# Performance work log

Hardware: AMD Instinct MI355X
Metric: run time of the kernel (lower is better)

The kernel has to match this reference:

```python
import jax, jax.numpy as jnp
import numpy as np


def _l2norm(x, eps=1e-6):
    return x / jnp.sqrt(jnp.sum(x * x, axis=-1, keepdims=True) + eps)


def setup_inputs() -> dict:
    key = jax.random.key(0)
    k1, k2, k3, k4 = jax.random.split(key, 4)
    b, h, L, dk, dv = 2, 8, 4096, 128, 128
    q = jax.random.normal(k1, (b, h, L, dk), jnp.float32)
    k = jax.random.normal(k2, (b, h, L, dk), jnp.float32)
    v = jax.random.normal(k3, (b, h, L, dv), jnp.float32)
    beta = jax.random.uniform(k4, (b, h, L), jnp.float32)  # sigmoid(b_proj) in module -> (0,1)
    return {"q": q, "k": k, "v": v, "beta": beta, "chunk_size": 32}


def _delta_rule_chunkwise(q, k, v, beta, chunk_size):
    b, h, L, dk = q.shape
    dv = v.shape[-1]
    c = chunk_size
    pad = (-L) % c
    if pad:
        q = jnp.pad(q, ((0, 0), (0, 0), (0, pad), (0, 0)))
        k = jnp.pad(k, ((0, 0), (0, 0), (0, pad), (0, 0)))
        v = jnp.pad(v, ((0, 0), (0, 0), (0, pad), (0, 0)))
        beta = jnp.pad(beta, ((0, 0), (0, 0), (0, pad)))
    Lp = L + pad
    n = Lp // c

    q = _l2norm(q)
    k = _l2norm(k)
    v = v * beta[..., None]
    kb = k * beta[..., None]

    # (b,h,n,c,d)
    resh = lambda t: t.reshape(b, h, n, c, t.shape[-1])
    q, k, v, kb = resh(q), resh(k), resh(v), resh(kb)

    tri = jnp.triu(jnp.ones((c, c), bool), 0)        # upper incl diag
    tri_s = jnp.triu(jnp.ones((c, c), bool), 1)      # strict upper

    # forward substitution: inv = (I + strictly-lower(k_beta k^T))^{-1}-style recurrence
    inv = -jnp.einsum('bhncd,bhned->bhnce', kb, k)
    inv = jnp.where(tri, 0.0, inv)
    for i in range(1, c):  # fixed small chunk_size loop (c=32)
        upd = jnp.einsum('bhnk,bhnkj->bhnj', inv[..., i, :], inv[..., :, :i])
        inv = inv.at[..., i, :i].add(upd)
    inv = inv + jnp.eye(c, dtype=inv.dtype)

    u = inv @ v    # (b,h,n,c,dv)
    w = inv @ kb   # (b,h,n,c,dk)

    # chunk-recurrent state scan over the n blocks
    qs = jnp.moveaxis(q, 2, 0)
    ks = jnp.moveaxis(k, 2, 0)
    us = jnp.moveaxis(u, 2, 0)
    ws = jnp.moveaxis(w, 2, 0)
    S0 = jnp.zeros((b, h, dk, dv), q.dtype)

    def step(S, blk):
        q_i, k_i, u_i, w_i = blk
        attn = jnp.einsum('bhcd,bhed->bhce', q_i, k_i)
        attn = jnp.where(tri_s, 0.0, attn)                       # causal within chunk
        u_i = u_i - jnp.einsum('bhcd,bhde->bhce', w_i, S)
        o_i = jnp.einsum('bhcd,bhde->bhce', q_i, S) + jnp.einsum('bhce,bhed->bhcd', attn, u_i)
        S = S + jnp.einsum('bhcd,bhce->bhde', k_i, u_i)
        return S, o_i

    S, out = jax.lax.scan(step, S0, (qs, ks, us, ws))
    out = jnp.moveaxis(out, 0, 2).reshape(b, h, Lp, dv)[:, :, :L]
    return out, S


def reference(q, k, v, beta, chunk_size):
    return _delta_rule_chunkwise(q, k, v, beta, int(chunk_size))
```

## Files before the change

kernel.cpp:

```cpp
#include <hip/hip_runtime.h>
#include <cstddef>

#define BH   16
#define LSEQ 4096
#define DK   128
#define DV   128
#define C    32
#define NCH  128
#define DVB  16
#define NDVB 8
#define PP   136
#define PC   40
#define PS   136
#define AP   33

#define RECSZ 22528
#define OQ    0
#define OWH   4096
#define OWL   8192
#define OKTH  12288
#define OKTL  16384
#define OATH  20480
#define OATL  21504

typedef __attribute__((ext_vector_type(4))) float f32x4;
typedef __attribute__((ext_vector_type(8))) short short8;
typedef __attribute__((ext_vector_type(4))) short s16x4;

__device__ inline unsigned split_bf16(float x) {
    unsigned u = __builtin_bit_cast(unsigned, x);
    unsigned r = u + 0x7fffu + ((u >> 16) & 1u);
    unsigned h = r >> 16;
    float hf = __builtin_bit_cast(float, r & 0xffff0000u);
    float res = x - hf;
    unsigned u2 = __builtin_bit_cast(unsigned, res);
    unsigned r2 = u2 + 0x7fffu + ((u2 >> 16) & 1u);
    return (h << 16) | (r2 >> 16);
}
__device__ inline short hi_bf16(float x) {
    unsigned u = __builtin_bit_cast(unsigned, x);
    return (short)((u + 0x7fffu + ((u >> 16) & 1u)) >> 16);
}
__device__ inline short trunc_bf16(float x) {
    return (short)(__builtin_bit_cast(unsigned, x) >> 16);
}

__device__ inline short8 fld(const short* P, int row0, int pitch, int k0, int lane) {
    return *(const short8*)(P + (row0 + (lane & 15)) * pitch + k0 + ((lane >> 4) << 3));
}
__device__ inline short8 fldz128(const short* P, int row0, int ks, int lane) {
    int row = row0 + (lane & 15);
    int c = ks * 4 + (lane >> 4);
    return *(const short8*)(P + row * 128 + ((c ^ (row & 7)) << 3));
}
__device__ inline short8 fldz32(const short* P, int row0, int lane) {
    int row = row0 + (lane & 15);
    int c = lane >> 4;
    return *(const short8*)(P + row * 32 + ((c ^ (row & 3)) << 3));
}
__device__ inline f32x4 mf(short8 a, short8 b, f32x4 c) {
    return __builtin_amdgcn_mfma_f32_16x16x32_bf16(a, b, c, 0, 0, 0);
}
__device__ inline void build_ifrags(int lane, short8& Iev, short8& Iod) {
    int n = lane & 15, q = lane >> 4;
#pragma unroll
    for (int j = 0; j < 8; ++j) {
        Iev[j] = (q * 8 + j == n)      ? (short)0x3F80 : (short)0;
        Iod[j] = (q * 8 + j == n + 16) ? (short)0x3F80 : (short)0;
    }
}
__device__ inline void store8_z128(short* Pg, int row, int col0, s16x4 v) {
    int c = col0 >> 3;
    *(s16x4*)(Pg + row * 128 + ((c ^ (row & 7)) << 3) + (col0 & 7)) = v;
}
__device__ inline void store8_z32(short* Pg, int row, int col0, s16x4 v) {
    int c = col0 >> 3;
    *(s16x4*)(Pg + row * 32 + ((c ^ (row & 3)) << 3) + (col0 & 7)) = v;
}
__device__ inline void dma1k(const short* g, short* l, int lane) {
    __builtin_amdgcn_global_load_lds(
        (const __attribute__((address_space(1))) unsigned int*)(g + lane * 8),
        (__attribute__((address_space(3))) unsigned int*)l, 16, 0, 0);
}

__global__ __launch_bounds__(256) void k_prep(const float* __restrict__ Q,
                                              const float* __restrict__ K,
                                              const float* __restrict__ V,
                                              const float* __restrict__ Beta,
                                              short* __restrict__ RECg,
                                              float* __restrict__ Uws) {
    __shared__ short knh[C * PP], knl[C * PP], vh[C * PP], vl[C * PP], qh[C * PP];
    __shared__ short knTh[DK * PC], knTl[DK * PC], vTh[DK * PC], vTl[DK * PC];
    __shared__ short Th[C * PC], Tl[C * PC];
    __shared__ float A[C * AP];
    __shared__ float sbeta[C];

    const int t = threadIdx.x, lane = t & 63, wv = t >> 6;
    const int quad = (t >> 4) & 3, l15 = t & 15;
    const int g = blockIdx.x;
    const size_t base = (size_t)g * (C * DK);
    short* rec = RECg + (size_t)g * RECSZ;
    short8 Iev, Iod;
    build_ifrags(lane, Iev, Iod);

    if (t < C) sbeta[t] = Beta[(size_t)(g >> 7) * LSEQ + (size_t)(g & 127) * C + t];

    const int sr = t >> 3, sc = (t & 7) * 16;
    f32x4 kk[4], vv[4], qq[4];
#pragma unroll
    for (int g4 = 0; g4 < 4; ++g4) {
        kk[g4] = *(const f32x4*)(K + base + 16 * t + 4 * g4);
        vv[g4] = *(const f32x4*)(V + base + 16 * t + 4 * g4);
        qq[g4] = *(const f32x4*)(Q + base + 16 * t + 4 * g4);
    }
    float ssk = 0.f, ssq = 0.f;
#pragma unroll
    for (int g4 = 0; g4 < 4; ++g4) {
#pragma unroll
        for (int e = 0; e < 4; ++e) {
            ssk += kk[g4][e] * kk[g4][e];
            ssq += qq[g4][e] * qq[g4][e];
        }
    }
    ssk += __shfl_xor(ssk, 1); ssk += __shfl_xor(ssk, 2); ssk += __shfl_xor(ssk, 4);
    ssq += __shfl_xor(ssq, 1); ssq += __shfl_xor(ssq, 2); ssq += __shfl_xor(ssq, 4);
    const float rk = rsqrtf(ssk + 1e-6f), rq = rsqrtf(ssq + 1e-6f);
#pragma unroll
    for (int half = 0; half < 2; ++half) {
        short8 h8, l8;
#pragma unroll
        for (int e = 0; e < 8; ++e) {
            unsigned p = split_bf16(kk[2 * half + (e >> 2)][e & 3] * rk);
            h8[e] = (short)(p >> 16); l8[e] = (short)(p & 0xffffu);
        }
        *(short8*)(knh + sr * PP + sc + 8 * half) = h8;
        *(short8*)(knl + sr * PP + sc + 8 * half) = l8;
#pragma unroll
        for (int e = 0; e < 8; ++e) {
            unsigned p = split_bf16(vv[2 * half + (e >> 2)][e & 3]);
            h8[e] = (short)(p >> 16); l8[e] = (short)(p & 0xffffu);
        }
        *(short8*)(vh + sr * PP + sc + 8 * half) = h8;
        *(short8*)(vl + sr * PP + sc + 8 * half) = l8;
        short8 q8;
#pragma unroll
        for (int e = 0; e < 8; ++e) q8[e] = hi_bf16(qq[2 * half + (e >> 2)][e & 3] * rq);
        *(short8*)(qh + sr * PP + sc + 8 * half) = q8;
        int c = (sc >> 3) + half;
        *(short8*)(rec + OQ + sr * 128 + ((c ^ (sr & 7)) << 3)) = q8;
    }
    __syncthreads();

    if (wv < 3) {
        const int a0 = (wv == 0) ? 0 : 16;
        const int b0 = (wv == 2) ? 16 : 0;
        f32x4 acc = {0.f, 0.f, 0.f, 0.f};
#pragma unroll
        for (int ks = 0; ks < 4; ++ks) {
            short8 ah = fld(knh, a0, PP, ks * 32, lane);
            short8 al = fld(knl, a0, PP, ks * 32, lane);
            short8 bh_ = fld(knh, b0, PP, ks * 32, lane);
            short8 bl_ = fld(knl, b0, PP, ks * 32, lane);
            acc = mf(ah, bh_, mf(ah, bl_, mf(al, bh_, acc)));
        }
#pragma unroll
        for (int r = 0; r < 4; ++r) {
            int row = a0 + quad * 4 + r, col = b0 + l15;
            A[row * AP + col] = (row > col) ? -sbeta[row] * acc[r] : 0.f;
        }
        f32x4 at = {0.f, 0.f, 0.f, 0.f};
#pragma unroll
        for (int ks = 0; ks < 4; ++ks) {
            short8 kh_ = fld(knh, b0, PP, ks * 32, lane);
            short8 kl_ = fld(knl, b0, PP, ks * 32, lane);
            short8 qf = fld(qh, a0, PP, ks * 32, lane);
            at = mf(kh_, qf, mf(kl_, qf, at));
        }
        s16x4 h4, l4;
#pragma unroll
        for (int r = 0; r < 4; ++r) {
            int cj = b0 + quad * 4 + r, ci = a0 + l15;
            float v = (cj <= ci) ? at[r] : 0.f;
            unsigned p = split_bf16(v);
            h4[r] = (short)(p >> 16); l4[r] = (short)(p & 0xffffu);
        }
        store8_z32(rec + OATH, a0 + l15, b0 + quad * 4, h4);
        store8_z32(rec + OATL, a0 + l15, b0 + quad * 4, l4);
    } else {
#pragma unroll
        for (int r = 0; r < 4; ++r) A[l15 * AP + 16 + quad * 4 + r] = 0.f;
        s16x4 z = {0, 0, 0, 0};
        store8_z32(rec + OATH, l15, 16 + quad * 4, z);
        store8_z32(rec + OATL, l15, 16 + quad * 4, z);
    }
    __syncthreads();

    auto tplane = [&](const short* src, short* dst, short* gdst) {
#pragma unroll
        for (int c0 = 0; c0 <= 16; c0 += 16) {
#pragma unroll
            for (int ks = 0; ks < 4; ++ks) {
                short8 fr = fld(src, c0, PP, ks * 32, lane);
                f32x4 z = {0.f, 0.f, 0.f, 0.f};
                f32x4 cA = mf(fr, Iev, z);
                f32x4 cB = mf(fr, Iod, z);
                s16x4 sA, sB;
#pragma unroll
                for (int r = 0; r < 4; ++r) { sA[r] = trunc_bf16(cA[r]); sB[r] = trunc_bf16(cB[r]); }
                *(s16x4*)(dst + (ks * 32 + l15) * PC + c0 + quad * 4) = sA;
                *(s16x4*)(dst + (ks * 32 + 16 + l15) * PC + c0 + quad * 4) = sB;
                if (gdst) {
                    store8_z32(gdst, ks * 32 + l15, c0 + quad * 4, sA);
                    store8_z32(gdst, ks * 32 + 16 + l15, c0 + quad * 4, sB);
                }
            }
        }
    };
    if (wv == 0) {
        tplane(knh, knTh, rec + OKTH);
        tplane(vl, vTl, nullptr);
    } else if (wv == 1) {
        tplane(knl, knTl, rec + OKTL);
    } else if (wv == 2) {
        tplane(vh, vTh, nullptr);
    } else if (lane < C) {
        const int j = lane;
        for (int i = 1; i < C; ++i) {
            float upd = 0.f;
            for (int kk2 = 1; kk2 < i; ++kk2) upd += A[i * AP + kk2] * A[kk2 * AP + j];
            if (j < i) A[i * AP + j] += upd;
        }
    }
    __syncthreads();

    {
        int tr = t >> 3, tc = (t & 7) * 4;
        s16x4 h4, l4;
#pragma unroll
        for (int e = 0; e < 4; ++e) {
            int j = tc + e;
            float val = ((tr == j) ? 1.f : (tr > j ? A[tr * AP + j] : 0.f)) * sbeta[j];
            unsigned p = split_bf16(val);
            h4[e] = (short)(p >> 16); l4[e] = (short)(p & 0xffffu);
        }
        *(s16x4*)(Th + tr * PC + tc) = h4;
        *(s16x4*)(Tl + tr * PC + tc) = l4;
    }
    __syncthreads();

    {
        const int ci0 = (wv & 1) * 16;
        short8 bTh = fld(Th, ci0, PC, 0, lane);
        short8 bTl = fld(Tl, ci0, PC, 0, lane);
        if (wv < 2) {
#pragma unroll
            for (int tt = 0; tt < 8; ++tt) {
                short8 ah = fld(vTh, tt * 16, PC, 0, lane);
                short8 al = fld(vTl, tt * 16, PC, 0, lane);
                f32x4 z = {0.f, 0.f, 0.f, 0.f};
                f32x4 acc = mf(ah, bTh, mf(ah, bTl, mf(al, bTh, z)));
                *(f32x4*)(Uws + (size_t)g * 4096 + (size_t)(ci0 + l15) * DK + tt * 16 + quad * 4) = acc;
            }
        } else {
#pragma unroll
            for (int tt = 0; tt < 8; ++tt) {
                short8 ah = fld(knTh, tt * 16, PC, 0, lane);
                short8 al = fld(knTl, tt * 16, PC, 0, lane);
                f32x4 z = {0.f, 0.f, 0.f, 0.f};
                f32x4 acc = mf(ah, bTh, mf(ah, bTl, mf(al, bTh, z)));
                s16x4 h4, l4;
#pragma unroll
                for (int r = 0; r < 4; ++r) {
                    unsigned p = split_bf16(acc[r]);
                    h4[r] = (short)(p >> 16); l4[r] = (short)(p & 0xffffu);
                }
                store8_z128(rec + OWH, ci0 + l15, tt * 16 + quad * 4, h4);
                store8_z128(rec + OWL, ci0 + l15, tt * 16 + quad * 4, l4);
            }
        }
    }
}

__global__ __launch_bounds__(512, 1) void k_scan(const short* __restrict__ RECg,
                                                 const float* __restrict__ Uws,
                                                 float* __restrict__ Out,
                                                 float* __restrict__ Sout) {
    __shared__ __attribute__((aligned(16))) short bALL[2][RECSZ];
    __shared__ short STh[DVB * PS], STl[DVB * PS];
    __shared__ short uTh[DVB * PC], uTl[DVB * PC];

    const int t = threadIdx.x, lane = t & 63, wv = t >> 6;
    const int quad = (t >> 4) & 3, l15 = t & 15;
    const int db = blockIdx.x >> 4, bhi = blockIdx.x & 15;
    const int vcol = db * DVB;
    const int r0 = (wv & 1) * 16;
    const int dk0 = wv * 16;
    const size_t gb = (size_t)bhi * NCH;

    f32x4 accS = {0.f, 0.f, 0.f, 0.f};
    float pu[4] = {0.f, 0.f, 0.f, 0.f};

    auto dma_chunk = [&](int cc, int s) {
        if (wv < 2) return;
        const short* src = RECg + (size_t)(gb + cc) * RECSZ;
        short* dst = bALL[s];
#pragma unroll
        for (int k = 0; k < 8; ++k) {
            int q = (wv - 2) + 6 * k;
            if (q < 44) dma1k(src + q * 512, dst + q * 512, lane);
        }
    };
    auto pref_u = [&](int cc) {
        if (wv < 2) {
            const size_t ub = (gb + cc) * 4096;
#pragma unroll
            for (int r = 0; r < 4; ++r)
                pu[r] = Uws[ub + (size_t)(r0 + quad * 4 + r) * DK + vcol + l15];
        }
    };

    for (int e = t; e < DVB * PS; e += 512) { STh[e] = 0; STl[e] = 0; }
    dma_chunk(0, 0);
    pref_u(0);
    __syncthreads();

    for (int cid = 0; cid < NCH; ++cid) {
        const int cur = cid & 1;
        const short* pC = bALL[cur];
        f32x4 oc = {0.f, 0.f, 0.f, 0.f};

        short8 kth = fldz32(pC + OKTH, dk0, lane);
        short8 ktl = fldz32(pC + OKTL, dk0, lane);
        short8 bah = {}, bal = {};

        if (wv >= 2) {
            if (cid + 1 < NCH) dma_chunk(cid + 1, cur ^ 1);
        } else {
            float p0 = pu[0], p1 = pu[1], p2 = pu[2], p3 = pu[3];
            if (cid + 1 < NCH) pref_u(cid + 1);

            f32x4 u0 = {-p0, -p1, -p2, -p3};
            f32x4 u1 = {0.f, 0.f, 0.f, 0.f}, u2 = {0.f, 0.f, 0.f, 0.f};
            f32x4 o1 = {0.f, 0.f, 0.f, 0.f};
#pragma unroll
            for (int ks = 0; ks < 4; ++ks) {
                short8 wh_ = fldz128(pC + OWH, r0, ks, lane);
                short8 wl_ = fldz128(pC + OWL, r0, ks, lane);
                short8 sh_ = fld(STh, 0, PS, ks * 32, lane);
                short8 sl_ = fld(STl, 0, PS, ks * 32, lane);
                short8 qf = fldz128(pC + OQ, r0, ks, lane);
                u0 = mf(wh_, sh_, u0);
                u1 = mf(wh_, sl_, u1);
                u2 = mf(wl_, sh_, u2);
                oc = mf(sh_, qf, oc);
                o1 = mf(sl_, qf, o1);
            }
            oc += o1;
            f32x4 us = u0 + u1 + u2;
            s16x4 h4, l4;
#pragma unroll
            for (int r = 0; r < 4; ++r) {
                unsigned p = split_bf16(-us[r]);
                h4[r] = (short)(p >> 16); l4[r] = (short)(p & 0xffffu);
            }
            *(s16x4*)(uTh + l15 * PC + r0 + quad * 4) = h4;
            *(s16x4*)(uTl + l15 * PC + r0 + quad * 4) = l4;
            bah = fldz32(pC + OATH, r0, lane);
            bal = fldz32(pC + OATL, r0, lane);
        }
        __syncthreads();

        short8 buh = fld(uTh, 0, PC, 0, lane);
        short8 bul = fld(uTl, 0, PC, 0, lane);
        if (wv < 2) {
            oc = mf(buh, bah, mf(buh, bal, mf(bul, bah, oc)));
            const size_t ob = ((size_t)bhi * LSEQ + (size_t)cid * C) * DK;
            *(f32x4*)(Out + ob + (size_t)(r0 + l15) * DK + vcol + quad * 4) = oc;
        }
        {
            f32x4 z = {0.f, 0.f, 0.f, 0.f};
            f32x4 tband = mf(kth, bul, mf(ktl, buh, z));
            accS = mf(kth, buh, accS);
            accS += tband;
            s16x4 h4, l4;
#pragma unroll
            for (int r = 0; r < 4; ++r) {
                unsigned p = split_bf16(accS[r]);
                h4[r] = (short)(p >> 16); l4[r] = (short)(p & 0xffffu);
            }
            *(s16x4*)(STh + l15 * PS + dk0 + quad * 4) = h4;
            *(s16x4*)(STl + l15 * PS + dk0 + quad * 4) = l4;
        }
        __syncthreads();
    }

#pragma unroll
    for (int r = 0; r < 4; ++r)
        Sout[(size_t)bhi * DK * DV + (size_t)(dk0 + quad * 4 + r) * DV + vcol + l15] = accS[r];
}

extern "C" void kernel_launch(void* const* d_in, const int* in_sizes, int n_in,
                              void* d_out, int out_size, void* d_ws, size_t ws_size,
                              hipStream_t stream) {
    const float* Q    = (const float*)d_in[0];
    const float* K    = (const float*)d_in[1];
    const float* V    = (const float*)d_in[2];
    const float* Beta = (const float*)d_in[3];

    float* Out  = (float*)d_out;
    float* Sout = Out + (size_t)BH * LSEQ * DV;

    short* RECg = (short*)d_ws;
    float* Uws  = (float*)(RECg + (size_t)BH * NCH * RECSZ);

    hipLaunchKernelGGL(k_prep, dim3(BH * NCH), dim3(256), 0, stream,
                       Q, K, V, Beta, RECg, Uws);
    hipLaunchKernelGGL(k_scan, dim3(BH * NDVB), dim3(512), 0, stream,
                       RECg, Uws, Out, Sout);
}
```

Before: 339.4 us.

## Pack U into the per-chunk record and offload the q·S product to idle waves

```diff
diff --git a/kernel.cpp b/kernel.cpp
--- a/kernel.cpp
+++ b/kernel.cpp
@@ -14,7 +14,7 @@
 #define PS   136
 #define AP   33
 
-#define RECSZ 22528
+#define RECSZ 30720
 #define OQ    0
 #define OWH   4096
 #define OWL   8192
@@ -22,6 +22,8 @@
 #define OKTL  16384
 #define OATH  20480
 #define OATL  21504
+#define OUH   22528
+#define OUL   26624
 
 typedef __attribute__((ext_vector_type(4))) float f32x4;
 typedef __attribute__((ext_vector_type(8))) short short8;
@@ -44,6 +46,9 @@
 __device__ inline short trunc_bf16(float x) {
     return (short)(__builtin_bit_cast(unsigned, x) >> 16);
 }
+__device__ inline float bf16_to_f(unsigned short s) {
+    return __builtin_bit_cast(float, ((unsigned)s) << 16);
+}
 
 __device__ inline short8 fld(const short* P, int row0, int pitch, int k0, int lane) {
     return *(const short8*)(P + (row0 + (lane & 15)) * pitch + k0 + ((lane >> 4) << 3));
@@ -87,8 +92,7 @@
                                               const float* __restrict__ K,
                                               const float* __restrict__ V,
                                               const float* __restrict__ Beta,
-                                              short* __restrict__ RECg,
-                                              float* __restrict__ Uws) {
+                                              short* __restrict__ RECg) {
     __shared__ short knh[C * PP], knl[C * PP], vh[C * PP], vl[C * PP], qh[C * PP];
     __shared__ short knTh[DK * PC], knTl[DK * PC], vTh[DK * PC], vTl[DK * PC];
     __shared__ short Th[C * PC], Tl[C * PC];
@@ -259,7 +263,14 @@
                 short8 al = fld(vTl, tt * 16, PC, 0, lane);
                 f32x4 z = {0.f, 0.f, 0.f, 0.f};
                 f32x4 acc = mf(ah, bTh, mf(ah, bTl, mf(al, bTh, z)));
-                *(f32x4*)(Uws + (size_t)g * 4096 + (size_t)(ci0 + l15) * DK + tt * 16 + quad * 4) = acc;
+                s16x4 h4, l4;
+#pragma unroll
+                for (int r = 0; r < 4; ++r) {
+                    unsigned p = split_bf16(acc[r]);
+                    h4[r] = (short)(p >> 16); l4[r] = (short)(p & 0xffffu);
+                }
+                store8_z128(rec + OUH, ci0 + l15, tt * 16 + quad * 4, h4);
+                store8_z128(rec + OUL, ci0 + l15, tt * 16 + quad * 4, l4);
             }
         } else {
 #pragma unroll
@@ -282,12 +293,12 @@
 }
 
 __global__ __launch_bounds__(512, 1) void k_scan(const short* __restrict__ RECg,
-                                                 const float* __restrict__ Uws,
                                                  float* __restrict__ Out,
                                                  float* __restrict__ Sout) {
     __shared__ __attribute__((aligned(16))) short bALL[2][RECSZ];
     __shared__ short STh[DVB * PS], STl[DVB * PS];
     __shared__ short uTh[DVB * PC], uTl[DVB * PC];
+    __shared__ float oP[2][16][20];
 
     const int t = threadIdx.x, lane = t & 63, wv = t >> 6;
     const int quad = (t >> 4) & 3, l15 = t & 15;
@@ -298,64 +309,75 @@
     const size_t gb = (size_t)bhi * NCH;
 
     f32x4 accS = {0.f, 0.f, 0.f, 0.f};
-    float pu[4] = {0.f, 0.f, 0.f, 0.f};
-
-    auto dma_chunk = [&](int cc, int s) {
-        if (wv < 2) return;
+    f32x4 ocp = {0.f, 0.f, 0.f, 0.f};
+
+    auto dma_rng = [&](int cc, int s, int q0, int n) {
         const short* src = RECg + (size_t)(gb + cc) * RECSZ;
         short* dst = bALL[s];
 #pragma unroll
-        for (int k = 0; k < 8; ++k) {
-            int q = (wv - 2) + 6 * k;
-            if (q < 44) dma1k(src + q * 512, dst + q * 512, lane);
-        }
+        for (int k = 0; k < 12; ++k)
+            if (k < n) dma1k(src + (q0 + k) * 512, dst + (q0 + k) * 512, lane);
     };
-    auto pref_u = [&](int cc) {
-        if (wv < 2) {
-            const size_t ub = (gb + cc) * 4096;
-#pragma unroll
-            for (int r = 0; r < 4; ++r)
-                pu[r] = Uws[ub + (size_t)(r0 + quad * 4 + r) * DK + vcol + l15];
-        }
-    };
 
     for (int e = t; e < DVB * PS; e += 512) { STh[e] = 0; STl[e] = 0; }
-    dma_chunk(0, 0);
-    pref_u(0);
+    if (wv >= 2) {
+        if (wv < 4) dma_rng(0, 0, (wv - 2) * 6, 6);
+        else        dma_rng(0, 0, 12 + (wv - 4) * 12, 12);
+    }
     __syncthreads();
 
     for (int cid = 0; cid < NCH; ++cid) {
         const int cur = cid & 1;
         const short* pC = bALL[cur];
-        f32x4 oc = {0.f, 0.f, 0.f, 0.f};
 
         short8 kth = fldz32(pC + OKTH, dk0, lane);
         short8 ktl = fldz32(pC + OKTL, dk0, lane);
         short8 bah = {}, bal = {};
 
-        if (wv >= 2) {
-            if (cid + 1 < NCH) dma_chunk(cid + 1, cur ^ 1);
+        if (wv >= 4) {
+            if (cid + 1 < NCH) dma_rng(cid + 1, cur ^ 1, 12 + (wv - 4) * 12, 12);
+        } else if (wv >= 2) {
+            short8 pSh[4], pSl[4], pQf[4];
+#pragma unroll
+            for (int ks = 0; ks < 4; ++ks) {
+                pSh[ks] = fld(STh, 0, PS, ks * 32, lane);
+                pSl[ks] = fld(STl, 0, PS, ks * 32, lane);
+                pQf[ks] = fldz128(pC + OQ, r0, ks, lane);
+            }
+            if (cid + 1 < NCH) dma_rng(cid + 1, cur ^ 1, (wv - 2) * 6, 6);
+            f32x4 oc = {0.f, 0.f, 0.f, 0.f}, o1 = {0.f, 0.f, 0.f, 0.f};
+#pragma unroll
+            for (int ks = 0; ks < 4; ++ks) {
+                oc = mf(pSh[ks], pQf[ks], oc);
+                o1 = mf(pSl[ks], pQf[ks], o1);
+            }
+            oc += o1;
+            *(f32x4*)(&oP[wv - 2][l15][quad * 4]) = oc;
         } else {
-            float p0 = pu[0], p1 = pu[1], p2 = pu[2], p3 = pu[3];
-            if (cid + 1 < NCH) pref_u(cid + 1);
-
-            f32x4 u0 = {-p0, -p1, -p2, -p3};
-            f32x4 u1 = {0.f, 0.f, 0.f, 0.f}, u2 = {0.f, 0.f, 0.f, 0.f};
-            f32x4 o1 = {0.f, 0.f, 0.f, 0.f};
+            if (cid > 0) {
+                const size_t ob = ((size_t)bhi * LSEQ + (size_t)(cid - 1) * C) * DK;
+                *(f32x4*)(Out + ob + (size_t)(r0 + l15) * DK + vcol + quad * 4) = ocp;
+            }
+            f32x4 u0, u1 = {0.f, 0.f, 0.f, 0.f}, u2 = {0.f, 0.f, 0.f, 0.f};
+            const int col = vcol + l15, cch = col >> 3, cc7 = col & 7;
+#pragma unroll
+            for (int r = 0; r < 4; ++r) {
+                int row = r0 + quad * 4 + r;
+                int off = row * 128 + ((cch ^ (row & 7)) << 3) + cc7;
+                float f = bf16_to_f(*(const unsigned short*)(pC + OUH + off)) +
+                          bf16_to_f(*(const unsigned short*)(pC + OUL + off));
+                u0[r] = -f;
+            }
 #pragma unroll
             for (int ks = 0; ks < 4; ++ks) {
                 short8 wh_ = fldz128(pC + OWH, r0, ks, lane);
                 short8 wl_ = fldz128(pC + OWL, r0, ks, lane);
                 short8 sh_ = fld(STh, 0, PS, ks * 32, lane);
                 short8 sl_ = fld(STl, 0, PS, ks * 32, lane);
-                short8 qf = fldz128(pC + OQ, r0, ks, lane);
                 u0 = mf(wh_, sh_, u0);
                 u1 = mf(wh_, sl_, u1);
                 u2 = mf(wl_, sh_, u2);
-                oc = mf(sh_, qf, oc);
-                o1 = mf(sl_, qf, o1);
-            }
-            oc += o1;
+            }
             f32x4 us = u0 + u1 + u2;
             s16x4 h4, l4;
 #pragma unroll
@@ -373,9 +395,9 @@
         short8 buh = fld(uTh, 0, PC, 0, lane);
         short8 bul = fld(uTl, 0, PC, 0, lane);
         if (wv < 2) {
+            f32x4 oc = *(const f32x4*)(&oP[wv][l15][quad * 4]);
             oc = mf(buh, bah, mf(buh, bal, mf(bul, bah, oc)));
-            const size_t ob = ((size_t)bhi * LSEQ + (size_t)cid * C) * DK;
-            *(f32x4*)(Out + ob + (size_t)(r0 + l15) * DK + vcol + quad * 4) = oc;
+            ocp = oc;
         }
         {
             f32x4 z = {0.f, 0.f, 0.f, 0.f};
@@ -392,6 +414,11 @@
             *(s16x4*)(STl + l15 * PS + dk0 + quad * 4) = l4;
         }
         __syncthreads();
+    }
+
+    if (wv < 2) {
+        const size_t ob = ((size_t)bhi * LSEQ + (size_t)(NCH - 1) * C) * DK;
+        *(f32x4*)(Out + ob + (size_t)(r0 + l15) * DK + vcol + quad * 4) = ocp;
     }
 
 #pragma unroll
@@ -411,10 +438,9 @@
     float* Sout = Out + (size_t)BH * LSEQ * DV;
 
     short* RECg = (short*)d_ws;
-    float* Uws  = (float*)(RECg + (size_t)BH * NCH * RECSZ);
 
     hipLaunchKernelGGL(k_prep, dim3(BH * NCH), dim3(256), 0, stream,
-                       Q, K, V, Beta, RECg, Uws);
+                       Q, K, V, Beta, RECg);
     hipLaunchKernelGGL(k_scan, dim3(BH * NDVB), dim3(512), 0, stream,
-                       RECg, Uws, Out, Sout);
-}
+                       RECg, Out, Sout);
+}
```

Result: slower. 361.4 us (+6.5%).

## Offload q·S output partial to DMA waves and defer output stores in scan

Applied to the files above, without the earlier changes.

```diff
diff --git a/kernel.cpp b/kernel.cpp
--- a/kernel.cpp
+++ b/kernel.cpp
@@ -81,6 +81,11 @@
     __builtin_amdgcn_global_load_lds(
         (const __attribute__((address_space(1))) unsigned int*)(g + lane * 8),
         (__attribute__((address_space(3))) unsigned int*)l, 16, 0, 0);
+}
+__device__ inline void bar_lgkm() {
+    asm volatile("s_waitcnt lgkmcnt(0)" ::: "memory");
+    __builtin_amdgcn_s_barrier();
+    asm volatile("" ::: "memory");
 }
 
 __global__ __launch_bounds__(256) void k_prep(const float* __restrict__ Q,
@@ -288,6 +293,7 @@
     __shared__ __attribute__((aligned(16))) short bALL[2][RECSZ];
     __shared__ short STh[DVB * PS], STl[DVB * PS];
     __shared__ short uTh[DVB * PC], uTl[DVB * PC];
+    __shared__ float oP[2][16][20];
 
     const int t = threadIdx.x, lane = t & 63, wv = t >> 6;
     const int quad = (t >> 4) & 3, l15 = t & 15;
@@ -298,17 +304,15 @@
     const size_t gb = (size_t)bhi * NCH;
 
     f32x4 accS = {0.f, 0.f, 0.f, 0.f};
+    f32x4 ocp = {0.f, 0.f, 0.f, 0.f};
     float pu[4] = {0.f, 0.f, 0.f, 0.f};
 
-    auto dma_chunk = [&](int cc, int s) {
-        if (wv < 2) return;
+    auto dma_rng = [&](int cc, int s, int q0, int n) {
         const short* src = RECg + (size_t)(gb + cc) * RECSZ;
         short* dst = bALL[s];
-#pragma unroll
-        for (int k = 0; k < 8; ++k) {
-            int q = (wv - 2) + 6 * k;
-            if (q < 44) dma1k(src + q * 512, dst + q * 512, lane);
-        }
+#pragma unroll 8
+        for (int k = 0; k < n; ++k)
+            dma1k(src + (q0 + k) * 512, dst + (q0 + k) * 512, lane);
     };
     auto pref_u = [&](int cc) {
         if (wv < 2) {
@@ -320,42 +324,57 @@
     };
 
     for (int e = t; e < DVB * PS; e += 512) { STh[e] = 0; STl[e] = 0; }
-    dma_chunk(0, 0);
+    if (wv >= 4)      dma_rng(0, 0, 12 + (wv - 4) * 8, 8);
+    else if (wv >= 2) dma_rng(0, 0, (wv - 2) * 6, 6);
     pref_u(0);
     __syncthreads();
 
     for (int cid = 0; cid < NCH; ++cid) {
         const int cur = cid & 1;
         const short* pC = bALL[cur];
-        f32x4 oc = {0.f, 0.f, 0.f, 0.f};
 
         short8 kth = fldz32(pC + OKTH, dk0, lane);
         short8 ktl = fldz32(pC + OKTL, dk0, lane);
         short8 bah = {}, bal = {};
 
-        if (wv >= 2) {
-            if (cid + 1 < NCH) dma_chunk(cid + 1, cur ^ 1);
+        if (wv >= 4) {
+            if (cid + 1 < NCH) dma_rng(cid + 1, cur ^ 1, 12 + (wv - 4) * 8, 8);
+        } else if (wv >= 2) {
+            short8 pSh[4], pSl[4], pQf[4];
+#pragma unroll
+            for (int ks = 0; ks < 4; ++ks) {
+                pSh[ks] = fld(STh, 0, PS, ks * 32, lane);
+                pSl[ks] = fld(STl, 0, PS, ks * 32, lane);
+                pQf[ks] = fldz128(pC + OQ, r0, ks, lane);
+            }
+            if (cid + 1 < NCH) dma_rng(cid + 1, cur ^ 1, (wv - 2) * 6, 6);
+            f32x4 z = {0.f, 0.f, 0.f, 0.f};
+            f32x4 oa = mf(pSh[0], pQf[0], z), ob_ = mf(pSl[0], pQf[0], z);
+            f32x4 oc2 = mf(pSh[1], pQf[1], z), od = mf(pSl[1], pQf[1], z);
+            oa = mf(pSh[2], pQf[2], oa); ob_ = mf(pSl[2], pQf[2], ob_);
+            oc2 = mf(pSh[3], pQf[3], oc2); od = mf(pSl[3], pQf[3], od);
+            f32x4 osum = (oa + ob_) + (oc2 + od);
+            *(f32x4*)(&oP[wv - 2][l15][quad * 4]) = osum;
         } else {
+            if (cid > 0) {
+                const size_t ob = ((size_t)bhi * LSEQ + (size_t)(cid - 1) * C) * DK;
+                *(f32x4*)(Out + ob + (size_t)(r0 + l15) * DK + vcol + quad * 4) = ocp;
+            }
             float p0 = pu[0], p1 = pu[1], p2 = pu[2], p3 = pu[3];
             if (cid + 1 < NCH) pref_u(cid + 1);
 
             f32x4 u0 = {-p0, -p1, -p2, -p3};
             f32x4 u1 = {0.f, 0.f, 0.f, 0.f}, u2 = {0.f, 0.f, 0.f, 0.f};
-            f32x4 o1 = {0.f, 0.f, 0.f, 0.f};
 #pragma unroll
             for (int ks = 0; ks < 4; ++ks) {
                 short8 wh_ = fldz128(pC + OWH, r0, ks, lane);
                 short8 wl_ = fldz128(pC + OWL, r0, ks, lane);
                 short8 sh_ = fld(STh, 0, PS, ks * 32, lane);
                 short8 sl_ = fld(STl, 0, PS, ks * 32, lane);
-                short8 qf = fldz128(pC + OQ, r0, ks, lane);
                 u0 = mf(wh_, sh_, u0);
                 u1 = mf(wh_, sl_, u1);
                 u2 = mf(wl_, sh_, u2);
-                oc = mf(sh_, qf, oc);
-                o1 = mf(sl_, qf, o1);
-            }
-            oc += o1;
+            }
             f32x4 us = u0 + u1 + u2;
             s16x4 h4, l4;
 #pragma unroll
@@ -368,20 +387,24 @@
             bah = fldz32(pC + OATH, r0, lane);
             bal = fldz32(pC + OATL, r0, lane);
         }
-        __syncthreads();
+        bar_lgkm();
 
         short8 buh = fld(uTh, 0, PC, 0, lane);
         short8 bul = fld(uTl, 0, PC, 0, lane);
         if (wv < 2) {
-            oc = mf(buh, bah, mf(buh, bal, mf(bul, bah, oc)));
-            const size_t ob = ((size_t)bhi * LSEQ + (size_t)cid * C) * DK;
-            *(f32x4*)(Out + ob + (size_t)(r0 + l15) * DK + vcol + quad * 4) = oc;
+            f32x4 oc = *(const f32x4*)(&oP[wv][l15][quad * 4]);
+            f32x4 z = {0.f, 0.f, 0.f, 0.f};
+            f32x4 m1 = mf(bul, bah, z);
+            f32x4 m2 = mf(buh, bal, z);
+            oc = mf(buh, bah, oc);
+            ocp = oc + m1 + m2;
         }
         {
             f32x4 z = {0.f, 0.f, 0.f, 0.f};
-            f32x4 tband = mf(kth, bul, mf(ktl, buh, z));
+            f32x4 ta = mf(ktl, buh, z);
+            f32x4 tb = mf(kth, bul, z);
             accS = mf(kth, buh, accS);
-            accS += tband;
+            accS += ta + tb;
             s16x4 h4, l4;
 #pragma unroll
             for (int r = 0; r < 4; ++r) {
@@ -391,7 +414,13 @@
             *(s16x4*)(STh + l15 * PS + dk0 + quad * 4) = h4;
             *(s16x4*)(STl + l15 * PS + dk0 + quad * 4) = l4;
         }
-        __syncthreads();
+        if (wv >= 2) asm volatile("s_waitcnt vmcnt(0)" ::: "memory");
+        bar_lgkm();
+    }
+
+    if (wv < 2) {
+        const size_t ob = ((size_t)bhi * LSEQ + (size_t)(NCH - 1) * C) * DK;
+        *(f32x4*)(Out + ob + (size_t)(r0 + l15) * DK + vcol + quad * 4) = ocp;
     }
 
 #pragma unroll
```

New measurement: 344.3 us. About the same (+1.4%).
